# Performance work log

Hardware: AMD Instinct MI355X
Metric: run time of the kernel (lower is better)

## Reference

```python
import jax, jax.numpy as jnp
import numpy as np

DIM = 384
HEADS = 8
RED = 2
WS = 8            # window size for Q
DWS = WS // 2     # window size for DWT-downsampled K/V
DIM_Q = DIM // RED
HEAD_D = DIM_Q // HEADS
SCALE = HEAD_D ** -0.5
B, H, W = 4, 256, 256


def setup_inputs() -> dict:
    key = jax.random.key(0)
    ks = jax.random.split(key, 5)
    x = jax.random.normal(ks[0], (B, DIM, H, W), dtype=jnp.float32)
    q_w = jax.random.normal(ks[1], (DIM_Q, DIM), dtype=jnp.float32) * 0.02
    # grouped 1x1 conv: Conv2d(4*DIM, 2*DIM_Q, groups=4) -> (out=2*DIM_Q, in_per_group=DIM)
    kv_w = jax.random.normal(ks[2], (2 * DIM_Q, DIM), dtype=jnp.float32) * 0.02
    proj_w = jax.random.normal(ks[3], (DIM, DIM_Q), dtype=jnp.float32) * 0.02
    proj_b = jax.random.normal(ks[4], (DIM,), dtype=jnp.float32) * 0.02
    return {"x": x, "q_w": q_w, "kv_w": kv_w, "proj_w": proj_w, "proj_b": proj_b}


def _dwt2d(x):
    # Haar DWT via 2x2 stride-2 grouped conv; output channel 4c+s = subband s of input channel c
    b, c, h, w = x.shape
    xr = x.reshape(b, c, h // 2, 2, w // 2, 2)
    a = xr[:, :, :, 0, :, 0]
    bb = xr[:, :, :, 0, :, 1]
    cc = xr[:, :, :, 1, :, 0]
    dd = xr[:, :, :, 1, :, 1]
    ll = 0.5 * (a + bb + cc + dd)
    lh = 0.5 * (-a - bb + cc + dd)
    hl = 0.5 * (-a + bb - cc + dd)
    hh = 0.5 * (a - bb - cc + dd)
    sub = jnp.stack([ll, lh, hl, hh], axis=2)  # (b, c, 4, h/2, w/2)
    return sub.reshape(b, 4 * c, h // 2, w // 2)


def _to_windows(f, ws, heads):
    # f: (b, heads*d, h, w) -> (b*nH*nW, heads, ws*ws, d)
    b, cq, h, w = f.shape
    d = cq // heads
    t = f.reshape(b, heads, d, h // ws, ws, w // ws, ws)
    t = t.transpose(0, 3, 5, 1, 4, 6, 2)  # (b, nH, nW, heads, ws, ws, d)
    return t.reshape(b * (h // ws) * (w // ws), heads, ws * ws, d)


def reference(x, q_w, kv_w, proj_w, proj_b):
    b, c, h, w = x.shape
    # Q path: 1x1 conv bottleneck
    q_feat = jnp.einsum('oc,bchw->bohw', q_w, x)
    # K/V path: DWT then grouped (g=4) 1x1 conv
    xd = _dwt2d(x)                                   # (b, 4c, h/2, w/2)
    xd_g = xd.reshape(b, 4, c, h // 2, w // 2)
    kv_wg = kv_w.reshape(4, (2 * DIM_Q) // 4, c)
    kv = jnp.einsum('goc,bgchw->bgohw', kv_wg, xd_g).reshape(b, 2 * DIM_Q, h // 2, w // 2)
    k_feat, v_feat = kv[:, :DIM_Q], kv[:, DIM_Q:]
    # window partition
    qw = _to_windows(q_feat, WS, HEADS)              # (nw, h, 64, d)
    kw = _to_windows(k_feat, DWS, HEADS)             # (nw, h, 16, d)
    vw = _to_windows(v_feat, DWS, HEADS)
    corr = jnp.einsum('whqd,whkd->whqk', qw, kw) * SCALE   # no softmax
    attn = jnp.einsum('whqk,whkd->whqd', corr, vw)         # (nw, heads, 64, d)
    # merge windows back: (b*nH*nW, heads, ws*ws, d) -> (b, heads*d, H, W)
    nH, nW = h // WS, w // WS
    t = attn.reshape(b, nH, nW, HEADS, WS, WS, HEAD_D)
    t = t.transpose(0, 3, 6, 1, 4, 2, 5)             # (b, heads, d, nH, ws, nW, ws)
    feat = t.reshape(b, DIM_Q, h, w)
    out = jnp.einsum('oc,bchw->bohw', proj_w, feat) + proj_b[None, :, None, None]
    return out
```

## Files before the change

kernel.cpp:

```cpp
#include <hip/hip_runtime.h>

#define DIM    384
#define DIM_Q  192
#define HEADS  8
#define HEAD_D 24
#define BATCH  4
#define HH     256
#define WW     256
#define NWIN   32
#define KVP    17
#define SCALE  0.20412414523193154f

__global__ __launch_bounds__(256) void wave_attn_fused(
    const float* __restrict__ x, const float* __restrict__ q_w,
    const float* __restrict__ kv_w, const float* __restrict__ proj_w,
    const float* __restrict__ proj_b, float* __restrict__ out)
{
    __shared__ float qbuf[96 * 64];
    __shared__ float kvbuf[DIM * KVP];
    __shared__ float xs[96 * 64];
    float* mbuf = xs;

    const int t = threadIdx.x;
    const int blk = ((int)blockIdx.x & 7) * 512 + ((int)blockIdx.x >> 3);
    const int b   = blk >> 10;
    const int wy  = (blk >> 5) & 31;
    const int wx  = blk & 31;
    const int by  = wy * 8, bx = wx * 8;

    const int tx = t & 15;
    const int ty = t >> 4;

    const int i2 = (tx >> 2) * 2;
    const int j2 = (tx & 3) * 2;

    float4 accq[12];
#pragma unroll
    for (int i = 0; i < 12; ++i) accq[i] = make_float4(0.f, 0.f, 0.f, 0.f);

    for (int g = 0; g < 4; ++g) {
#pragma unroll
        for (int k = 0; k < 6; ++k) {
            int idx = t + (k << 8);
            int f  = idx & 1;
            int pi = (idx >> 1) & 7;
            int cl = idx >> 4;
            const float4 v = *(const float4*)(
                x + (((size_t)(b * DIM + g * 96 + cl) * HH + by + pi) * WW + bx + f * 4));
            *(float4*)&xs[cl * 64 + pi * 8 + f * 4] = v;
        }
        __syncthreads();

        for (int c4 = 0; c4 < 24; ++c4) {
            const float4 xv0 = *(const float4*)&xs[(c4 * 4 + 0) * 64 + tx * 4];
            const float4 xv1 = *(const float4*)&xs[(c4 * 4 + 1) * 64 + tx * 4];
            const float4 xv2 = *(const float4*)&xs[(c4 * 4 + 2) * 64 + tx * 4];
            const float4 xv3 = *(const float4*)&xs[(c4 * 4 + 3) * 64 + tx * 4];
#pragma unroll
            for (int i = 0; i < 12; ++i) {
                const float4 w = *(const float4*)(q_w + (ty + 16 * i) * DIM + g * 96 + c4 * 4);
                accq[i].x += w.x * xv0.x + w.y * xv1.x + w.z * xv2.x + w.w * xv3.x;
                accq[i].y += w.x * xv0.y + w.y * xv1.y + w.z * xv2.y + w.w * xv3.y;
                accq[i].z += w.x * xv0.z + w.y * xv1.z + w.z * xv2.z + w.w * xv3.z;
                accq[i].w += w.x * xv0.w + w.y * xv1.w + w.z * xv2.w + w.w * xv3.w;
            }
        }

        {
            float acck[6] = {0.f, 0.f, 0.f, 0.f, 0.f, 0.f};
            for (int cl = 0; cl < 96; ++cl) {
                const float2 ab = *(const float2*)&xs[cl * 64 + i2 * 8 + j2];
                const float2 cd = *(const float2*)&xs[cl * 64 + (i2 + 1) * 8 + j2];
                const float a  = ab.x, bb = ab.y;
                const float cv = cd.x, dv = cd.y;
                const float ll = 0.5f * (a + bb + cv + dv);
                const float lh = 0.5f * (cv + dv - a - bb);
                const float hl = 0.5f * (bb + dv - a - cv);
                const float hh = 0.5f * (a + dv - bb - cv);
#pragma unroll
                for (int rr = 0; rr < 6; ++rr) {
                    const float4 w = *(const float4*)(kv_w + (g * 96 + ty * 6 + rr) * DIM + cl * 4);
                    acck[rr] += w.x * ll + w.y * lh + w.z * hl + w.w * hh;
                }
            }
#pragma unroll
            for (int rr = 0; rr < 6; ++rr)
                kvbuf[(g * 96 + ty * 6 + rr) * KVP + tx] = acck[rr];
        }
        __syncthreads();
    }

    if (t < DIM_Q) {
        const int h = t / 24, d1 = t % 24;
        float kvals[16];
#pragma unroll
        for (int p = 0; p < 16; ++p) kvals[p] = kvbuf[t * KVP + p];
        for (int d2 = 0; d2 < 24; ++d2) {
            float s = 0.f;
#pragma unroll
            for (int p = 0; p < 16; ++p)
                s += kvals[p] * kvbuf[(DIM_Q + h * 24 + d2) * KVP + p];
            mbuf[(h * 24 + d1) * 24 + d2] = SCALE * s;
        }
    }
    __syncthreads();

    float4 acco[24];
#pragma unroll
    for (int i = 0; i < 24; ++i) acco[i] = make_float4(0.f, 0.f, 0.f, 0.f);

#pragma unroll
    for (int r = 0; r < 2; ++r) {
#pragma unroll
        for (int ii = 0; ii < 6; ++ii)
            *(float4*)&qbuf[(ty + 16 * ii) * 64 + tx * 4] = accq[ii + 6 * r];
        __syncthreads();

        float4 featacc[6];
#pragma unroll
        for (int ii = 0; ii < 6; ++ii) {
            const int ch = 96 * r + ty + 16 * ii;
            const int h  = ch / 24, d = ch % 24;
            const int hl = (h - 4 * r) * 24;
            float4 acc = make_float4(0.f, 0.f, 0.f, 0.f);
            for (int dp = 0; dp < 24; ++dp) {
                const float4 qv = *(const float4*)&qbuf[(hl + dp) * 64 + tx * 4];
                const float m = mbuf[(h * 24 + dp) * 24 + d];
                acc.x += m * qv.x; acc.y += m * qv.y;
                acc.z += m * qv.z; acc.w += m * qv.w;
            }
            featacc[ii] = acc;
        }
        __syncthreads();
#pragma unroll
        for (int ii = 0; ii < 6; ++ii)
            *(float4*)&qbuf[(ty + 16 * ii) * 64 + tx * 4] = featacc[ii];
        __syncthreads();

        for (int c4 = 0; c4 < 24; ++c4) {
            const float4 f0 = *(const float4*)&qbuf[(c4 * 4 + 0) * 64 + tx * 4];
            const float4 f1 = *(const float4*)&qbuf[(c4 * 4 + 1) * 64 + tx * 4];
            const float4 f2 = *(const float4*)&qbuf[(c4 * 4 + 2) * 64 + tx * 4];
            const float4 f3 = *(const float4*)&qbuf[(c4 * 4 + 3) * 64 + tx * 4];
#pragma unroll
            for (int i = 0; i < 24; ++i) {
                const float4 w = *(const float4*)(proj_w + (ty + 16 * i) * DIM_Q + 96 * r + c4 * 4);
                acco[i].x += w.x * f0.x + w.y * f1.x + w.z * f2.x + w.w * f3.x;
                acco[i].y += w.x * f0.y + w.y * f1.y + w.z * f2.y + w.w * f3.y;
                acco[i].z += w.x * f0.z + w.y * f1.z + w.z * f2.z + w.w * f3.z;
                acco[i].w += w.x * f0.w + w.y * f1.w + w.z * f2.w + w.w * f3.w;
            }
        }
        __syncthreads();
    }

    const int pi = tx >> 1;
    const int pj = (tx & 1) * 4;
#pragma unroll
    for (int i = 0; i < 24; ++i) {
        const int o = ty + 16 * i;
        const float bias = proj_b[o];
        float4 r = acco[i];
        r.x += bias; r.y += bias; r.z += bias; r.w += bias;
        *(float4*)(out + (((size_t)(b * DIM + o) * HH + by + pi) * WW + bx + pj)) = r;
    }
}

extern "C" void kernel_launch(void* const* d_in, const int* in_sizes, int n_in,
                              void* d_out, int out_size, void* d_ws, size_t ws_size,
                              hipStream_t stream) {
    const float* x      = (const float*)d_in[0];
    const float* q_w    = (const float*)d_in[1];
    const float* kv_w   = (const float*)d_in[2];
    const float* proj_w = (const float*)d_in[3];
    const float* proj_b = (const float*)d_in[4];
    float* out = (float*)d_out;
    (void)in_sizes; (void)n_in; (void)out_size; (void)d_ws; (void)ws_size;

    dim3 grid(BATCH * NWIN * NWIN);
    dim3 block(256);
    hipLaunchKernelGGL(wave_attn_fused, grid, block, 0, stream,
                       x, q_w, kv_w, proj_w, proj_b, out);
}
```

Before: 3.492 ms.

## Double block size, prefetch next channel group, precompute DWT in shared memory

Raises the block to 512 threads, so each thread holds half the Q and output accumulators, which lowers register pressure. The next 96-channel slice of x is prefetched into registers while the current slice is computed, and the Haar DWT is applied once in place in shared memory instead of being recomputed inside the KV loop. The attention and projection stages now use a full-size second shared buffer and run in a single pass instead of two halves. The cost is more shared memory per block and extra barriers, which may limit how many blocks fit on a CU.

```diff
diff --git a/kernel.cpp b/kernel.cpp
--- a/kernel.cpp
+++ b/kernel.cpp
@@ -2,21 +2,19 @@
 
 #define DIM    384
 #define DIM_Q  192
-#define HEADS  8
-#define HEAD_D 24
 #define BATCH  4
 #define HH     256
 #define WW     256
-#define NWIN   32
 #define KVP    17
 #define SCALE  0.20412414523193154f
 
-__global__ __launch_bounds__(256) void wave_attn_fused(
+__global__ __launch_bounds__(512) void wave_attn_fused(
     const float* __restrict__ x, const float* __restrict__ q_w,
     const float* __restrict__ kv_w, const float* __restrict__ proj_w,
     const float* __restrict__ proj_b, float* __restrict__ out)
 {
-    __shared__ float qbuf[96 * 64];
+    __shared__ float qbuf[DIM_Q * 64];
+    __shared__ float fbuf[DIM_Q * 64];
     __shared__ float kvbuf[DIM * KVP];
     __shared__ float xs[96 * 64];
     float* mbuf = xs;
@@ -31,25 +29,40 @@
     const int tx = t & 15;
     const int ty = t >> 4;
 
-    const int i2 = (tx >> 2) * 2;
-    const int j2 = (tx & 3) * 2;
-
-    float4 accq[12];
-#pragma unroll
-    for (int i = 0; i < 12; ++i) accq[i] = make_float4(0.f, 0.f, 0.f, 0.f);
+    float4 accq[6];
+#pragma unroll
+    for (int i = 0; i < 6; ++i) accq[i] = make_float4(0.f, 0.f, 0.f, 0.f);
+
+#pragma unroll
+    for (int k = 0; k < 3; ++k) {
+        const int idx = t + (k << 9);
+        const int f  = idx & 1;
+        const int pi = (idx >> 1) & 7;
+        const int cl = idx >> 4;
+        *(float4*)&xs[cl * 64 + pi * 8 + f * 4] = *(const float4*)(
+            x + (((size_t)(b * DIM + cl) * HH + by + pi) * WW + bx + f * 4));
+    }
+    __syncthreads();
 
     for (int g = 0; g < 4; ++g) {
-#pragma unroll
-        for (int k = 0; k < 6; ++k) {
-            int idx = t + (k << 8);
-            int f  = idx & 1;
-            int pi = (idx >> 1) & 7;
-            int cl = idx >> 4;
-            const float4 v = *(const float4*)(
-                x + (((size_t)(b * DIM + g * 96 + cl) * HH + by + pi) * WW + bx + f * 4));
-            *(float4*)&xs[cl * 64 + pi * 8 + f * 4] = v;
-        }
-        __syncthreads();
+        float4 pf0, pf1, pf2;
+        if (g < 3) {
+            {
+                const int idx = t;
+                const int f = idx & 1, pi = (idx >> 1) & 7, cl = idx >> 4;
+                pf0 = *(const float4*)(x + (((size_t)(b * DIM + (g + 1) * 96 + cl) * HH + by + pi) * WW + bx + f * 4));
+            }
+            {
+                const int idx = t + 512;
+                const int f = idx & 1, pi = (idx >> 1) & 7, cl = idx >> 4;
+                pf1 = *(const float4*)(x + (((size_t)(b * DIM + (g + 1) * 96 + cl) * HH + by + pi) * WW + bx + f * 4));
+            }
+            {
+                const int idx = t + 1024;
+                const int f = idx & 1, pi = (idx >> 1) & 7, cl = idx >> 4;
+                pf2 = *(const float4*)(x + (((size_t)(b * DIM + (g + 1) * 96 + cl) * HH + by + pi) * WW + bx + f * 4));
+            }
+        }
 
         for (int c4 = 0; c4 < 24; ++c4) {
             const float4 xv0 = *(const float4*)&xs[(c4 * 4 + 0) * 64 + tx * 4];
@@ -57,108 +70,146 @@
             const float4 xv2 = *(const float4*)&xs[(c4 * 4 + 2) * 64 + tx * 4];
             const float4 xv3 = *(const float4*)&xs[(c4 * 4 + 3) * 64 + tx * 4];
 #pragma unroll
-            for (int i = 0; i < 12; ++i) {
-                const float4 w = *(const float4*)(q_w + (ty + 16 * i) * DIM + g * 96 + c4 * 4);
+            for (int i = 0; i < 6; ++i) {
+                const float4 w = *(const float4*)(q_w + (ty + 32 * i) * DIM + g * 96 + c4 * 4);
                 accq[i].x += w.x * xv0.x + w.y * xv1.x + w.z * xv2.x + w.w * xv3.x;
                 accq[i].y += w.x * xv0.y + w.y * xv1.y + w.z * xv2.y + w.w * xv3.y;
                 accq[i].z += w.x * xv0.z + w.y * xv1.z + w.z * xv2.z + w.w * xv3.z;
                 accq[i].w += w.x * xv0.w + w.y * xv1.w + w.z * xv2.w + w.w * xv3.w;
             }
         }
+        __syncthreads();
+
+        if (t < 384) {
+            const int base = (t >> 2) * 64 + (t & 3) * 16;
+            const float4 r0a = *(const float4*)&xs[base + 0];
+            const float4 r0b = *(const float4*)&xs[base + 4];
+            const float4 r1a = *(const float4*)&xs[base + 8];
+            const float4 r1b = *(const float4*)&xs[base + 12];
+            float4 o0, o1, o2, o3;
+            o0.x = 0.5f * ( r0a.x + r0a.y + r1a.x + r1a.y);
+            o0.y = 0.5f * (-r0a.x - r0a.y + r1a.x + r1a.y);
+            o0.z = 0.5f * (-r0a.x + r0a.y - r1a.x + r1a.y);
+            o0.w = 0.5f * ( r0a.x - r0a.y - r1a.x + r1a.y);
+            o1.x = 0.5f * ( r0a.z + r0a.w + r1a.z + r1a.w);
+            o1.y = 0.5f * (-r0a.z - r0a.w + r1a.z + r1a.w);
+            o1.z = 0.5f * (-r0a.z + r0a.w - r1a.z + r1a.w);
+            o1.w = 0.5f * ( r0a.z - r0a.w - r1a.z + r1a.w);
+            o2.x = 0.5f * ( r0b.x + r0b.y + r1b.x + r1b.y);
+            o2.y = 0.5f * (-r0b.x - r0b.y + r1b.x + r1b.y);
+            o2.z = 0.5f * (-r0b.x + r0b.y - r1b.x + r1b.y);
+            o2.w = 0.5f * ( r0b.x - r0b.y - r1b.x + r1b.y);
+            o3.x = 0.5f * ( r0b.z + r0b.w + r1b.z + r1b.w);
+            o3.y = 0.5f * (-r0b.z - r0b.w + r1b.z + r1b.w);
+            o3.z = 0.5f * (-r0b.z + r0b.w - r1b.z + r1b.w);
+            o3.w = 0.5f * ( r0b.z - r0b.w - r1b.z + r1b.w);
+            *(float4*)&xs[base + 0]  = o0;
+            *(float4*)&xs[base + 4]  = o1;
+            *(float4*)&xs[base + 8]  = o2;
+            *(float4*)&xs[base + 12] = o3;
+        }
+        __syncthreads();
 
         {
-            float acck[6] = {0.f, 0.f, 0.f, 0.f, 0.f, 0.f};
+            float acck0 = 0.f, acck1 = 0.f, acck2 = 0.f;
+            const float* kw = kv_w + (size_t)(g * 96 + ty * 3) * DIM;
             for (int cl = 0; cl < 96; ++cl) {
-                const float2 ab = *(const float2*)&xs[cl * 64 + i2 * 8 + j2];
-                const float2 cd = *(const float2*)&xs[cl * 64 + (i2 + 1) * 8 + j2];
-                const float a  = ab.x, bb = ab.y;
-                const float cv = cd.x, dv = cd.y;
-                const float ll = 0.5f * (a + bb + cv + dv);
-                const float lh = 0.5f * (cv + dv - a - bb);
-                const float hl = 0.5f * (bb + dv - a - cv);
-                const float hh = 0.5f * (a + dv - bb - cv);
-#pragma unroll
-                for (int rr = 0; rr < 6; ++rr) {
-                    const float4 w = *(const float4*)(kv_w + (g * 96 + ty * 6 + rr) * DIM + cl * 4);
-                    acck[rr] += w.x * ll + w.y * lh + w.z * hl + w.w * hh;
-                }
-            }
-#pragma unroll
-            for (int rr = 0; rr < 6; ++rr)
-                kvbuf[(g * 96 + ty * 6 + rr) * KVP + tx] = acck[rr];
+                const float4 d  = *(const float4*)&xs[cl * 64 + tx * 4];
+                const float4 w0 = *(const float4*)(kw + cl * 4);
+                const float4 w1 = *(const float4*)(kw + DIM + cl * 4);
+                const float4 w2 = *(const float4*)(kw + 2 * DIM + cl * 4);
+                acck0 += w0.x * d.x + w0.y * d.y + w0.z * d.z + w0.w * d.w;
+                acck1 += w1.x * d.x + w1.y * d.y + w1.z * d.z + w1.w * d.w;
+                acck2 += w2.x * d.x + w2.y * d.y + w2.z * d.z + w2.w * d.w;
+            }
+            kvbuf[(g * 96 + ty * 3 + 0) * KVP + tx] = acck0;
+            kvbuf[(g * 96 + ty * 3 + 1) * KVP + tx] = acck1;
+            kvbuf[(g * 96 + ty * 3 + 2) * KVP + tx] = acck2;
         }
         __syncthreads();
-    }
-
-    if (t < DIM_Q) {
-        const int h = t / 24, d1 = t % 24;
+
+        if (g < 3) {
+            {
+                const int idx = t;
+                const int f = idx & 1, pi = (idx >> 1) & 7, cl = idx >> 4;
+                *(float4*)&xs[cl * 64 + pi * 8 + f * 4] = pf0;
+            }
+            {
+                const int idx = t + 512;
+                const int f = idx & 1, pi = (idx >> 1) & 7, cl = idx >> 4;
+                *(float4*)&xs[cl * 64 + pi * 8 + f * 4] = pf1;
+            }
+            {
+                const int idx = t + 1024;
+                const int f = idx & 1, pi = (idx >> 1) & 7, cl = idx >> 4;
+                *(float4*)&xs[cl * 64 + pi * 8 + f * 4] = pf2;
+            }
+            __syncthreads();
+        }
+    }
+
+#pragma unroll
+    for (int i = 0; i < 6; ++i)
+        *(float4*)&qbuf[(ty + 32 * i) * 64 + tx * 4] = accq[i];
+
+    if (t < 384) {
+        const int hd1   = t >> 1;
+        const int h     = hd1 / 24;
+        const int dbase = (t & 1) * 12;
         float kvals[16];
 #pragma unroll
-        for (int p = 0; p < 16; ++p) kvals[p] = kvbuf[t * KVP + p];
-        for (int d2 = 0; d2 < 24; ++d2) {
+        for (int p = 0; p < 16; ++p) kvals[p] = kvbuf[hd1 * KVP + p];
+        const float* vrow = &kvbuf[(DIM_Q + h * 24 + dbase) * KVP];
+        for (int d2 = 0; d2 < 12; ++d2) {
             float s = 0.f;
 #pragma unroll
             for (int p = 0; p < 16; ++p)
-                s += kvals[p] * kvbuf[(DIM_Q + h * 24 + d2) * KVP + p];
-            mbuf[(h * 24 + d1) * 24 + d2] = SCALE * s;
+                s += kvals[p] * vrow[d2 * KVP + p];
+            mbuf[hd1 * 24 + dbase + d2] = SCALE * s;
         }
     }
     __syncthreads();
 
-    float4 acco[24];
-#pragma unroll
-    for (int i = 0; i < 24; ++i) acco[i] = make_float4(0.f, 0.f, 0.f, 0.f);
-
-#pragma unroll
-    for (int r = 0; r < 2; ++r) {
-#pragma unroll
-        for (int ii = 0; ii < 6; ++ii)
-            *(float4*)&qbuf[(ty + 16 * ii) * 64 + tx * 4] = accq[ii + 6 * r];
-        __syncthreads();
-
-        float4 featacc[6];
-#pragma unroll
-        for (int ii = 0; ii < 6; ++ii) {
-            const int ch = 96 * r + ty + 16 * ii;
-            const int h  = ch / 24, d = ch % 24;
-            const int hl = (h - 4 * r) * 24;
-            float4 acc = make_float4(0.f, 0.f, 0.f, 0.f);
-            for (int dp = 0; dp < 24; ++dp) {
-                const float4 qv = *(const float4*)&qbuf[(hl + dp) * 64 + tx * 4];
-                const float m = mbuf[(h * 24 + dp) * 24 + d];
-                acc.x += m * qv.x; acc.y += m * qv.y;
-                acc.z += m * qv.z; acc.w += m * qv.w;
-            }
-            featacc[ii] = acc;
-        }
-        __syncthreads();
-#pragma unroll
-        for (int ii = 0; ii < 6; ++ii)
-            *(float4*)&qbuf[(ty + 16 * ii) * 64 + tx * 4] = featacc[ii];
-        __syncthreads();
-
-        for (int c4 = 0; c4 < 24; ++c4) {
-            const float4 f0 = *(const float4*)&qbuf[(c4 * 4 + 0) * 64 + tx * 4];
-            const float4 f1 = *(const float4*)&qbuf[(c4 * 4 + 1) * 64 + tx * 4];
-            const float4 f2 = *(const float4*)&qbuf[(c4 * 4 + 2) * 64 + tx * 4];
-            const float4 f3 = *(const float4*)&qbuf[(c4 * 4 + 3) * 64 + tx * 4];
-#pragma unroll
-            for (int i = 0; i < 24; ++i) {
-                const float4 w = *(const float4*)(proj_w + (ty + 16 * i) * DIM_Q + 96 * r + c4 * 4);
-                acco[i].x += w.x * f0.x + w.y * f1.x + w.z * f2.x + w.w * f3.x;
-                acco[i].y += w.x * f0.y + w.y * f1.y + w.z * f2.y + w.w * f3.y;
-                acco[i].z += w.x * f0.z + w.y * f1.z + w.z * f2.z + w.w * f3.z;
-                acco[i].w += w.x * f0.w + w.y * f1.w + w.z * f2.w + w.w * f3.w;
-            }
-        }
-        __syncthreads();
+#pragma unroll
+    for (int ii = 0; ii < 6; ++ii) {
+        const int ch = ty + 32 * ii;
+        const int h = ch / 24, d = ch % 24;
+        const float* qrow = &qbuf[h * 24 * 64 + tx * 4];
+        const float* mcol = &mbuf[h * 24 * 24 + d];
+        float4 acc = make_float4(0.f, 0.f, 0.f, 0.f);
+        for (int dp = 0; dp < 24; ++dp) {
+            const float4 qv = *(const float4*)(qrow + dp * 64);
+            const float  m  = mcol[dp * 24];
+            acc.x += m * qv.x; acc.y += m * qv.y;
+            acc.z += m * qv.z; acc.w += m * qv.w;
+        }
+        *(float4*)&fbuf[ch * 64 + tx * 4] = acc;
+    }
+    __syncthreads();
+
+    float4 acco[12];
+#pragma unroll
+    for (int i = 0; i < 12; ++i) acco[i] = make_float4(0.f, 0.f, 0.f, 0.f);
+    for (int c4 = 0; c4 < 48; ++c4) {
+        const float4 f0 = *(const float4*)&fbuf[(c4 * 4 + 0) * 64 + tx * 4];
+        const float4 f1 = *(const float4*)&fbuf[(c4 * 4 + 1) * 64 + tx * 4];
+        const float4 f2 = *(const float4*)&fbuf[(c4 * 4 + 2) * 64 + tx * 4];
+        const float4 f3 = *(const float4*)&fbuf[(c4 * 4 + 3) * 64 + tx * 4];
+#pragma unroll
+        for (int i = 0; i < 12; ++i) {
+            const float4 w = *(const float4*)(proj_w + (ty + 32 * i) * DIM_Q + c4 * 4);
+            acco[i].x += w.x * f0.x + w.y * f1.x + w.z * f2.x + w.w * f3.x;
+            acco[i].y += w.x * f0.y + w.y * f1.y + w.z * f2.y + w.w * f3.y;
+            acco[i].z += w.x * f0.z + w.y * f1.z + w.z * f2.z + w.w * f3.z;
+            acco[i].w += w.x * f0.w + w.y * f1.w + w.z * f2.w + w.w * f3.w;
+        }
     }
 
     const int pi = tx >> 1;
     const int pj = (tx & 1) * 4;
 #pragma unroll
-    for (int i = 0; i < 24; ++i) {
-        const int o = ty + 16 * i;
+    for (int i = 0; i < 12; ++i) {
+        const int o = ty + 32 * i;
         const float bias = proj_b[o];
         float4 r = acco[i];
         r.x += bias; r.y += bias; r.z += bias; r.w += bias;
@@ -177,8 +228,8 @@
     float* out = (float*)d_out;
     (void)in_sizes; (void)n_in; (void)out_size; (void)d_ws; (void)ws_size;
 
-    dim3 grid(BATCH * NWIN * NWIN);
-    dim3 block(256);
+    dim3 grid(BATCH * 32 * 32);
+    dim3 block(512);
     hipLaunchKernelGGL(wave_attn_fused, grid, block, 0, stream,
                        x, q_w, kv_w, proj_w, proj_b, out);
 }
```

New measurement: 2.924 ms. 16.3% less time.
